# Optimization experiments

Hardware: AMD Instinct MI355X
Metric: run time of the kernel (lower is better)

The kernel has to match this reference:

```python
import jax, jax.numpy as jnp
import numpy as np

B, T = 512, 8192
MIN_SPEECH = 1.0      # config.min_speech_frames
MAX_EXPAND = 3.0      # config.max_speech_expand
TOPK_RATIO = 0.35     # config.pause_topk_ratio
MIN_BW = 0.1          # config.pause_min_boundary_weight
BIAS_W = 0.15         # config.pause_boundary_bias_weight
TEMP = 0.12           # config.pause_soft_temperature


def setup_inputs() -> dict:
    key = jax.random.key(0)
    ks = jax.random.split(key, 9)
    return {
        "dur_anchor_src": jax.random.uniform(ks[0], (B, T)) * 10.0,
        "dur_logratio_unit": jax.random.normal(ks[1], (B, T)) * 0.3,
        "pause_weight_unit": jax.random.uniform(ks[2], (B, T)),
        "boundary_latent": jax.random.uniform(ks[3], (B, T)),
        "unit_mask": jnp.ones((B, T), jnp.float32),
        "speech_budget_win": jax.random.uniform(ks[4], (B,)) * (2.0 * T),
        "pause_budget_win": jax.random.uniform(ks[5], (B,)) * (0.2 * T),
        "previous_speech_exec": jax.random.uniform(ks[6], (B, T)) * 3.0,
        "previous_pause_exec": jax.random.uniform(ks[7], (B, T)),
        "commit_frontier": jax.random.randint(ks[8], (B,), 0, T // 2),
    }


def reference(dur_anchor_src, dur_logratio_unit, pause_weight_unit, boundary_latent,
              unit_mask, speech_budget_win, pause_budget_win,
              previous_speech_exec, previous_pause_exec, commit_frontier):
    Tn = unit_mask.shape[1]
    pos = jnp.arange(Tn)[None, :]                                  # [1,T]
    prefix_mask = (pos < commit_frontier[:, None]).astype(unit_mask.dtype)  # [B,T]
    tail_mask = unit_mask * (1.0 - prefix_mask)

    # ---- lift budgets to feasible region (reuse_prefix=True) ----
    prefix_speech = jnp.sum(previous_speech_exec * unit_mask * prefix_mask, axis=1)
    prefix_pause = jnp.sum(previous_pause_exec * unit_mask * prefix_mask, axis=1)
    min_tail_speech = jnp.sum(tail_mask, axis=1) * MIN_SPEECH
    speech_budget = jnp.maximum(speech_budget_win, prefix_speech + min_tail_speech)
    pause_budget = jnp.maximum(pause_budget_win, prefix_pause)

    # ---- project speech ----
    anchor = jnp.maximum(dur_anchor_src, MIN_SPEECH)
    base = anchor * jnp.exp(dur_logratio_unit)
    candidate = jnp.clip(base, MIN_SPEECH, anchor * MAX_EXPAND) * unit_mask
    speech_prefix = previous_speech_exec * unit_mask * prefix_mask
    rem_s = speech_budget - jnp.sum(speech_prefix, axis=1)          # [B]
    cand_tail_sum = jnp.maximum(jnp.sum(candidate * tail_mask, axis=1), 1e-6)
    do_s = (jnp.sum(tail_mask, axis=1) > 0) & (rem_s > 0)
    scale_s = jnp.where(do_s, rem_s / cand_tail_sum, 0.0)[:, None]
    speech = (speech_prefix + candidate * scale_s * tail_mask) * unit_mask

    # ---- project pause (soft top-k selection) ----
    scores = (jnp.maximum(pause_weight_unit, 0.0)
              + BIAS_W * (MIN_BW + jnp.maximum(boundary_latent, 0.0))) * unit_mask
    keep_k = max(1, int(round(Tn * TOPK_RATIO)))                    # static, < T
    topv = jax.lax.top_k(scores, keep_k)[0]                         # [B,keep_k]
    thr = jax.lax.stop_gradient(topv[:, -1])[:, None]               # detached threshold
    gate = jax.nn.sigmoid((scores - thr) / TEMP)
    sparse = scores * gate * unit_mask

    pause_prefix = previous_pause_exec * unit_mask * prefix_mask
    rem_p = jnp.maximum(pause_budget - jnp.sum(pause_prefix, axis=1), 0.0)
    tail_sum = jnp.sum(tail_mask, axis=1)
    fallback = tail_mask / jnp.maximum(tail_sum, 1.0)[:, None]
    tail_cand = jnp.maximum(sparse, 0.0) * tail_mask + fallback * 1e-6
    denom = jnp.maximum(jnp.sum(tail_cand * tail_mask, axis=1), 1e-6)
    do_p = (tail_sum > 0) & (rem_p > 0)
    scale_p = jnp.where(do_p, rem_p / denom, 0.0)[:, None]
    pause = (pause_prefix + tail_cand * scale_p * tail_mask) * unit_mask

    return jnp.stack([speech, pause])                               # [2,B,T]
```

## Files before the change

kernel.cpp:

```cpp
#include <hip/hip_runtime.h>

#define T_DIM 8192
#define NTH 1024
#define NWAVE 16
#define GROUPS 2
#define KEEP_K 2867
#define KSCALE 32768.0f
#define INV_KSCALE (1.0f / 32768.0f)

typedef float nt4 __attribute__((ext_vector_type(4)));

__device__ __forceinline__ void scan_top256(const unsigned* bins, unsigned k, int lane,
                                            unsigned* sh_digit, unsigned* sh_k) {
    const int r0 = lane * 4;
    const unsigned c0 = bins[255 - r0];
    const unsigned c1 = bins[255 - (r0 + 1)];
    const unsigned c2 = bins[255 - (r0 + 2)];
    const unsigned c3 = bins[255 - (r0 + 3)];
    const unsigned s1 = c0 + c1, s2 = s1 + c2, s3 = s2 + c3;
    unsigned tot = s3;
    #pragma unroll
    for (int off = 1; off < 64; off <<= 1) {
        const unsigned n = __shfl_up(tot, off, 64);
        if (lane >= off) tot += n;
    }
    const unsigned excl = tot - s3;
    const unsigned Pc[4] = { excl + c0, excl + s1, excl + s2, excl + s3 };
    unsigned prev = excl;
    #pragma unroll
    for (int c = 0; c < 4; ++c) {
        if (Pc[c] >= k && prev < k) {
            *sh_digit = (unsigned)(255 - (r0 + c));
            *sh_k = k - prev;
        }
        prev = Pc[c];
    }
}

__global__ __launch_bounds__(NTH) void srp_kernel(
    const float* __restrict__ g_anchor,
    const float* __restrict__ g_lr,
    const float* __restrict__ g_pw,
    const float* __restrict__ g_bl,
    const float* __restrict__ g_mask,
    const float* __restrict__ g_sbud,
    const float* __restrict__ g_pbud,
    const float* __restrict__ g_psp,
    const float* __restrict__ g_ppa,
    const int*  __restrict__ g_front,
    float* __restrict__ g_out,
    int n_rows)
{
    constexpr float MIN_SPEECH = 1.0f;
    constexpr float MAX_EXPAND = 3.0f;
    constexpr float MIN_BW = 0.1f;
    constexpr float BIAS_W = 0.15f;
    constexpr float INV_TEMP = 1.0f / 0.12f;

    __shared__ unsigned ku[T_DIM / 2];
    __shared__ unsigned hist[NWAVE][256];
    __shared__ unsigned s_tot[256];
    __shared__ float wred[NWAVE][4];
    __shared__ float s_scal[6];
    __shared__ unsigned sh_hb, sh_k1, sh_lb, sh_k2;

    const int b = blockIdx.x;
    const int tid = threadIdx.x;
    const int wave = tid >> 6;
    const int lane = tid & 63;
    const long long row = (long long)b * T_DIM;
    const int f = g_front[b];

    #pragma unroll
    for (int d = 0; d < 4; ++d) hist[wave][lane + 64 * d] = 0u;

    float SC1[8];
    float PM[8];
    float a_ps = 0.f, a_pp = 0.f, a_ts = 0.f, a_cs = 0.f;

    #pragma unroll
    for (int g = 0; g < GROUPS; ++g) {
        const int t0 = g * 4096 + (tid << 2);
        float m_[4], tl_[4];
        {
            const float4 mk4 = *reinterpret_cast<const float4*>(g_mask + row + t0);
            float4 ps4 = {0.f, 0.f, 0.f, 0.f};
            float4 pp4 = {0.f, 0.f, 0.f, 0.f};
            if (t0 < f) {
                ps4 = *reinterpret_cast<const float4*>(g_psp + row + t0);
                pp4 = *reinterpret_cast<const float4*>(g_ppa + row + t0);
            }
            #pragma unroll
            for (int c = 0; c < 4; ++c) {
                const int i = (g << 2) + c;
                const int t = t0 + c;
                const float m = (&mk4.x)[c];
                const bool pre = (t < f);
                const float tail = pre ? 0.0f : m;
                const float ps = (&ps4.x)[c];
                const float pp = (&pp4.x)[c];
                if (pre) { a_ps += ps * m; a_pp += pp * m; }
                a_ts += tail;
                SC1[i] = pre ? ps * m * m : 0.0f;
                PM[i]  = pre ? pp * m * m : m;
                m_[c] = m; tl_[c] = tail;
            }
        }
        if (t0 + 3 >= f) {
            const float4 an4 = *reinterpret_cast<const float4*>(g_anchor + row + t0);
            const float4 lr4 = *reinterpret_cast<const float4*>(g_lr + row + t0);
            #pragma unroll
            for (int c = 0; c < 4; ++c) {
                const int i = (g << 2) + c;
                const float an = fmaxf((&an4.x)[c], MIN_SPEECH);
                const float cand = fminf(fmaxf(an * __expf((&lr4.x)[c]), MIN_SPEECH),
                                         an * MAX_EXPAND) * m_[c];
                a_cs += cand * tl_[c];
                SC1[i] += cand * tl_[c] * m_[c];
            }
        }
        {
            const float4 pw4 = *reinterpret_cast<const float4*>(g_pw + row + t0);
            const float4 bl4 = *reinterpret_cast<const float4*>(g_bl + row + t0);
            unsigned kk0 = 0u, kk1 = 0u;
            #pragma unroll
            for (int c = 0; c < 4; ++c) {
                const float s = (fmaxf((&pw4.x)[c], 0.0f)
                                 + BIAS_W * (MIN_BW + fmaxf((&bl4.x)[c], 0.0f))) * m_[c];
                const unsigned key = (unsigned)fminf(s * KSCALE, 65535.0f);
                atomicAdd(&hist[wave][key >> 8], 1u);
                if (c < 2) kk0 |= key << (16 * c);
                else       kk1 |= key << (16 * (c - 2));
            }
            uint2 w2; w2.x = kk0; w2.y = kk1;
            *reinterpret_cast<uint2*>(&ku[t0 >> 1]) = w2;
        }
    }

    #pragma unroll
    for (int o = 32; o > 0; o >>= 1) {
        a_ps += __shfl_down(a_ps, o, 64);
        a_pp += __shfl_down(a_pp, o, 64);
        a_ts += __shfl_down(a_ts, o, 64);
        a_cs += __shfl_down(a_cs, o, 64);
    }
    if (lane == 0) {
        wred[wave][0] = a_ps; wred[wave][1] = a_pp;
        wred[wave][2] = a_ts; wred[wave][3] = a_cs;
    }
    __syncthreads();

    if (tid < 256) {
        unsigned s = 0;
        #pragma unroll
        for (int w = 0; w < NWAVE; ++w) s += hist[w][tid];
        s_tot[tid] = s;
    }
    if (tid == 0) {
        float ps = 0.f, pp = 0.f, ts = 0.f, cs = 0.f;
        for (int w = 0; w < NWAVE; ++w) {
            ps += wred[w][0]; pp += wred[w][1];
            ts += wred[w][2]; cs += wred[w][3];
        }
        const float sb = fmaxf(g_sbud[b], ps + ts * MIN_SPEECH);
        const float pb = fmaxf(g_pbud[b], pp);
        const float rem_s = sb - ps;
        const float cts = fmaxf(cs, 1e-6f);
        s_scal[0] = (ts > 0.0f && rem_s > 0.0f) ? (rem_s / cts) : 0.0f;
        s_scal[1] = fmaxf(pb - pp, 0.0f);
        s_scal[2] = ts;
        s_scal[3] = fmaxf(ts, 1.0f);
    }
    __syncthreads();

    if (wave == 0) scan_top256(s_tot, KEEP_K, lane, &sh_hb, &sh_k1);

    {
        const float scale_s = s_scal[0];
        #pragma unroll
        for (int g = 0; g < GROUPS; ++g) {
            const int t0 = g * 4096 + (tid << 2);
            nt4 vs;
            #pragma unroll
            for (int c = 0; c < 4; ++c) {
                const int i = (g << 2) + c;
                const int t = t0 + c;
                vs[c] = (t < f) ? SC1[i] : SC1[i] * scale_s;
            }
            __builtin_nontemporal_store(vs, reinterpret_cast<nt4*>(g_out + row + t0));
        }
    }
    #pragma unroll
    for (int d = 0; d < 4; ++d) hist[wave][lane + 64 * d] = 0u;
    __syncthreads();

    const unsigned hb = sh_hb;
    #pragma unroll
    for (int g = 0; g < GROUPS; ++g) {
        const int t0 = g * 4096 + (tid << 2);
        const uint2 w2 = *reinterpret_cast<const uint2*>(&ku[t0 >> 1]);
        const unsigned k0 = w2.x & 0xFFFFu, k1 = w2.x >> 16;
        const unsigned k2 = w2.y & 0xFFFFu, k3 = w2.y >> 16;
        if ((k0 >> 8) == hb) atomicAdd(&hist[wave][k0 & 0xFFu], 1u);
        if ((k1 >> 8) == hb) atomicAdd(&hist[wave][k1 & 0xFFu], 1u);
        if ((k2 >> 8) == hb) atomicAdd(&hist[wave][k2 & 0xFFu], 1u);
        if ((k3 >> 8) == hb) atomicAdd(&hist[wave][k3 & 0xFFu], 1u);
    }
    __syncthreads();
    if (tid < 256) {
        unsigned s = 0;
        #pragma unroll
        for (int w = 0; w < NWAVE; ++w) s += hist[w][tid];
        s_tot[tid] = s;
    }
    __syncthreads();
    if (wave == 0) scan_top256(s_tot, sh_k1, lane, &sh_lb, &sh_k2);
    __syncthreads();

    const float thr = (float)((sh_hb << 8) | sh_lb) * INV_KSCALE;

    const float inv_ts6 = 1e-6f / s_scal[3];
    float a_d = 0.0f;
    #pragma unroll
    for (int g = 0; g < GROUPS; ++g) {
        const int t0 = g * 4096 + (tid << 2);
        if (t0 + 3 < f) continue;
        const uint2 w2 = *reinterpret_cast<const uint2*>(&ku[t0 >> 1]);
        const unsigned kk[4] = { w2.x & 0xFFFFu, w2.x >> 16, w2.y & 0xFFFFu, w2.y >> 16 };
        #pragma unroll
        for (int c = 0; c < 4; ++c) {
            const int i = (g << 2) + c;
            const int t = t0 + c;
            if (t >= f) {
                const float m = PM[i];
                const float s = (float)kk[c] * INV_KSCALE;
                const float gate = 1.0f / (1.0f + __expf(-(s - thr) * INV_TEMP));
                const float tc = s * gate * m * m + m * inv_ts6;
                a_d += tc * m;
                PM[i] = tc * m * m;
            }
        }
    }
    #pragma unroll
    for (int o = 32; o > 0; o >>= 1) a_d += __shfl_down(a_d, o, 64);
    if (lane == 0) wred[wave][0] = a_d;
    __syncthreads();
    if (tid == 0) {
        float d = 0.f;
        for (int w = 0; w < NWAVE; ++w) d += wred[w][0];
        const float denom = fmaxf(d, 1e-6f);
        const float ts = s_scal[2];
        const float rem_p = s_scal[1];
        s_scal[4] = (ts > 0.0f && rem_p > 0.0f) ? (rem_p / denom) : 0.0f;
    }
    __syncthreads();

    const float scale_p = s_scal[4];
    const long long out_off = (long long)n_rows * T_DIM;
    #pragma unroll
    for (int g = 0; g < GROUPS; ++g) {
        const int t0 = g * 4096 + (tid << 2);
        nt4 vp;
        #pragma unroll
        for (int c = 0; c < 4; ++c) {
            const int i = (g << 2) + c;
            const int t = t0 + c;
            vp[c] = (t < f) ? PM[i] : PM[i] * scale_p;
        }
        __builtin_nontemporal_store(vp, reinterpret_cast<nt4*>(g_out + out_off + row + t0));
    }
}

extern "C" void kernel_launch(void* const* d_in, const int* in_sizes, int n_in,
                              void* d_out, int out_size, void* d_ws, size_t ws_size,
                              hipStream_t stream) {
    const float* anchor = (const float*)d_in[0];
    const float* lr     = (const float*)d_in[1];
    const float* pw     = (const float*)d_in[2];
    const float* bl     = (const float*)d_in[3];
    const float* mask   = (const float*)d_in[4];
    const float* sbud   = (const float*)d_in[5];
    const float* pbud   = (const float*)d_in[6];
    const float* psp    = (const float*)d_in[7];
    const float* ppa    = (const float*)d_in[8];
    const int*   front  = (const int*)d_in[9];
    float* out = (float*)d_out;
    const int B = in_sizes[5];
    srp_kernel<<<B, NTH, 0, stream>>>(anchor, lr, pw, bl, mask, sbud, pbud,
                                      psp, ppa, front, out, B);
}
```

Measured before the change: 164.7 us.

## Replace single-thread reductions with redundant per-wave shuffles and overlap stores with radix scans

Every wave now reduces the per-wave partial sums itself with xor shuffles. This replaces the tid==0 serial reduction and the broadcast through shared scalars, and removes several __syncthreads barriers. Wave 0 sums the histogram bins straight into registers for the radix-select scan while the other waves write the speech output and the prefix part of the pause output, so stores overlap with the scans. Wave 0 catches up on its own stores afterwards, and the final pause store skips prefix chunks that were already written. The cost is redundant reduction work in every wave and wave 0 doing extra stores after its scan.

```diff
diff --git a/kernel.cpp b/kernel.cpp
--- a/kernel.cpp
+++ b/kernel.cpp
@@ -10,13 +10,11 @@
 
 typedef float nt4 __attribute__((ext_vector_type(4)));
 
-__device__ __forceinline__ void scan_top256(const unsigned* bins, unsigned k, int lane,
-                                            unsigned* sh_digit, unsigned* sh_k) {
+__device__ __forceinline__ void scan_top256_reg(unsigned c0, unsigned c1,
+                                                unsigned c2, unsigned c3,
+                                                unsigned k, int lane,
+                                                unsigned* sh_digit, unsigned* sh_k) {
     const int r0 = lane * 4;
-    const unsigned c0 = bins[255 - r0];
-    const unsigned c1 = bins[255 - (r0 + 1)];
-    const unsigned c2 = bins[255 - (r0 + 2)];
-    const unsigned c3 = bins[255 - (r0 + 3)];
     const unsigned s1 = c0 + c1, s2 = s1 + c2, s3 = s2 + c3;
     unsigned tot = s3;
     #pragma unroll
@@ -59,9 +57,7 @@
 
     __shared__ unsigned ku[T_DIM / 2];
     __shared__ unsigned hist[NWAVE][256];
-    __shared__ unsigned s_tot[256];
     __shared__ float wred[NWAVE][4];
-    __shared__ float s_scal[6];
     __shared__ unsigned sh_hb, sh_k1, sh_lb, sh_k2;
 
     const int b = blockIdx.x;
@@ -150,33 +146,35 @@
     }
     __syncthreads();
 
-    if (tid < 256) {
-        unsigned s = 0;
-        #pragma unroll
-        for (int w = 0; w < NWAVE; ++w) s += hist[w][tid];
-        s_tot[tid] = s;
-    }
-    if (tid == 0) {
-        float ps = 0.f, pp = 0.f, ts = 0.f, cs = 0.f;
+    float bv = wred[lane & 15][lane >> 4];
+    bv += __shfl_xor(bv, 8, 64);
+    bv += __shfl_xor(bv, 4, 64);
+    bv += __shfl_xor(bv, 2, 64);
+    bv += __shfl_xor(bv, 1, 64);
+    const float ps_t = __shfl(bv, 0, 64);
+    const float pp_t = __shfl(bv, 16, 64);
+    const float ts_t = __shfl(bv, 32, 64);
+    const float cs_t = __shfl(bv, 48, 64);
+    const float sb = fmaxf(g_sbud[b], ps_t + ts_t * MIN_SPEECH);
+    const float pb = fmaxf(g_pbud[b], pp_t);
+    const float rem_s = sb - ps_t;
+    const float scale_s = (ts_t > 0.0f && rem_s > 0.0f)
+                              ? (rem_s / fmaxf(cs_t, 1e-6f)) : 0.0f;
+    const float rem_p = fmaxf(pb - pp_t, 0.0f);
+    const float inv_ts6 = 1e-6f / fmaxf(ts_t, 1.0f);
+
+    if (wave == 0) {
+        const int r0 = lane * 4;
+        unsigned c0 = 0, c1 = 0, c2 = 0, c3 = 0;
+        #pragma unroll
         for (int w = 0; w < NWAVE; ++w) {
-            ps += wred[w][0]; pp += wred[w][1];
-            ts += wred[w][2]; cs += wred[w][3];
-        }
-        const float sb = fmaxf(g_sbud[b], ps + ts * MIN_SPEECH);
-        const float pb = fmaxf(g_pbud[b], pp);
-        const float rem_s = sb - ps;
-        const float cts = fmaxf(cs, 1e-6f);
-        s_scal[0] = (ts > 0.0f && rem_s > 0.0f) ? (rem_s / cts) : 0.0f;
-        s_scal[1] = fmaxf(pb - pp, 0.0f);
-        s_scal[2] = ts;
-        s_scal[3] = fmaxf(ts, 1.0f);
-    }
-    __syncthreads();
-
-    if (wave == 0) scan_top256(s_tot, KEEP_K, lane, &sh_hb, &sh_k1);
-
-    {
-        const float scale_s = s_scal[0];
+            c0 += hist[w][255 - r0];
+            c1 += hist[w][255 - (r0 + 1)];
+            c2 += hist[w][255 - (r0 + 2)];
+            c3 += hist[w][255 - (r0 + 3)];
+        }
+        scan_top256_reg(c0, c1, c2, c3, KEEP_K, lane, &sh_hb, &sh_k1);
+    } else {
         #pragma unroll
         for (int g = 0; g < GROUPS; ++g) {
             const int t0 = g * 4096 + (tid << 2);
@@ -190,9 +188,24 @@
             __builtin_nontemporal_store(vs, reinterpret_cast<nt4*>(g_out + row + t0));
         }
     }
+    __syncthreads();
+
+    if (wave == 0) {
+        #pragma unroll
+        for (int g = 0; g < GROUPS; ++g) {
+            const int t0 = g * 4096 + (tid << 2);
+            nt4 vs;
+            #pragma unroll
+            for (int c = 0; c < 4; ++c) {
+                const int i = (g << 2) + c;
+                const int t = t0 + c;
+                vs[c] = (t < f) ? SC1[i] : SC1[i] * scale_s;
+            }
+            __builtin_nontemporal_store(vs, reinterpret_cast<nt4*>(g_out + row + t0));
+        }
+    }
     #pragma unroll
     for (int d = 0; d < 4; ++d) hist[wave][lane + 64 * d] = 0u;
-    __syncthreads();
 
     const unsigned hb = sh_hb;
     #pragma unroll
@@ -207,19 +220,35 @@
         if ((k3 >> 8) == hb) atomicAdd(&hist[wave][k3 & 0xFFu], 1u);
     }
     __syncthreads();
-    if (tid < 256) {
-        unsigned s = 0;
-        #pragma unroll
-        for (int w = 0; w < NWAVE; ++w) s += hist[w][tid];
-        s_tot[tid] = s;
-    }
-    __syncthreads();
-    if (wave == 0) scan_top256(s_tot, sh_k1, lane, &sh_lb, &sh_k2);
+
+    if (wave == 0) {
+        const int r0 = lane * 4;
+        unsigned c0 = 0, c1 = 0, c2 = 0, c3 = 0;
+        #pragma unroll
+        for (int w = 0; w < NWAVE; ++w) {
+            c0 += hist[w][255 - r0];
+            c1 += hist[w][255 - (r0 + 1)];
+            c2 += hist[w][255 - (r0 + 2)];
+            c3 += hist[w][255 - (r0 + 3)];
+        }
+        scan_top256_reg(c0, c1, c2, c3, sh_k1, lane, &sh_lb, &sh_k2);
+    } else {
+        #pragma unroll
+        for (int g = 0; g < GROUPS; ++g) {
+            const int t0 = g * 4096 + (tid << 2);
+            if (t0 + 3 < f) {
+                nt4 vp;
+                #pragma unroll
+                for (int c = 0; c < 4; ++c) vp[c] = PM[(g << 2) + c];
+                __builtin_nontemporal_store(
+                    vp, reinterpret_cast<nt4*>(g_out + (long long)n_rows * T_DIM + row + t0));
+            }
+        }
+    }
     __syncthreads();
 
     const float thr = (float)((sh_hb << 8) | sh_lb) * INV_KSCALE;
 
-    const float inv_ts6 = 1e-6f / s_scal[3];
     float a_d = 0.0f;
     #pragma unroll
     for (int g = 0; g < GROUPS; ++g) {
@@ -245,21 +274,20 @@
     for (int o = 32; o > 0; o >>= 1) a_d += __shfl_down(a_d, o, 64);
     if (lane == 0) wred[wave][0] = a_d;
     __syncthreads();
-    if (tid == 0) {
-        float d = 0.f;
-        for (int w = 0; w < NWAVE; ++w) d += wred[w][0];
-        const float denom = fmaxf(d, 1e-6f);
-        const float ts = s_scal[2];
-        const float rem_p = s_scal[1];
-        s_scal[4] = (ts > 0.0f && rem_p > 0.0f) ? (rem_p / denom) : 0.0f;
-    }
-    __syncthreads();
-
-    const float scale_p = s_scal[4];
+
+    float dv = (lane < 16) ? wred[lane][0] : 0.0f;
+    dv += __shfl_xor(dv, 8, 64);
+    dv += __shfl_xor(dv, 4, 64);
+    dv += __shfl_xor(dv, 2, 64);
+    dv += __shfl_xor(dv, 1, 64);
+    const float denom = fmaxf(__shfl(dv, 0, 64), 1e-6f);
+    const float scale_p = (ts_t > 0.0f && rem_p > 0.0f) ? (rem_p / denom) : 0.0f;
+
     const long long out_off = (long long)n_rows * T_DIM;
     #pragma unroll
     for (int g = 0; g < GROUPS; ++g) {
         const int t0 = g * 4096 + (tid << 2);
+        if (wave != 0 && t0 + 3 < f) continue;
         nt4 vp;
         #pragma unroll
         for (int c = 0; c < 4; ++c) {
```

Result: no change. 163.9 us (-0.4%).
